# Kernel tuning notes

Hardware: AMD Instinct MI355X
Metric: run time of the kernel (lower is better)

## Reference

```python
import jax, jax.numpy as jnp
import numpy as np
import math

B, T, C = 4, 2048, 1024
N_HEAD = 16
HEAD_DIM = C // N_HEAD


def setup_inputs() -> dict:
    key = jax.random.key(0)
    k1, k2, k3, k4, k5 = jax.random.split(key, 5)
    s = 1.0 / math.sqrt(C)
    return {
        "x": jax.random.normal(k1, (B, T, C), dtype=jnp.float32),
        "W_attn": jax.random.normal(k2, (3 * C, C), dtype=jnp.float32) * s,
        "b_attn": jax.random.normal(k3, (3 * C,), dtype=jnp.float32) * 0.02,
        "W_proj": jax.random.normal(k4, (C, C), dtype=jnp.float32) * s,
        "b_proj": jax.random.normal(k5, (C,), dtype=jnp.float32) * 0.02,
    }


def reference(x, W_attn, b_attn, W_proj, b_proj):
    Bx, Tx, Cx = x.shape
    # QKV projection (torch Linear: x @ W.T + b), split into q,k,v
    qkv = jnp.einsum("btc,dc->btd", x, W_attn) + b_attn  # [B,T,3C]
    q, k, v = jnp.split(qkv, 3, axis=-1)
    # [B,T,C] -> [B,H,T,hd]
    def to_heads(t):
        return t.reshape(Bx, Tx, N_HEAD, HEAD_DIM).transpose(0, 2, 1, 3)
    q, k, v = to_heads(q), to_heads(k), to_heads(v)
    scale = 1.0 / math.sqrt(HEAD_DIM)
    att = jnp.einsum("bhqd,bhkd->bhqk", q, k) * scale  # [B,H,T,T]
    causal = jnp.tril(jnp.ones((Tx, Tx), dtype=bool))
    att = jnp.where(causal, att, -jnp.inf)
    att = jax.nn.softmax(att, axis=-1)
    y = jnp.einsum("bhqk,bhkd->bhqd", att, v)  # [B,H,T,hd]
    y = y.transpose(0, 2, 1, 3).reshape(Bx, Tx, Cx)
    y = jnp.einsum("btc,dc->btd", y, W_proj) + b_proj
    return y
```

## Files before the change

### kernel.cpp

```cpp
#include <hip/hip_runtime.h>
#include <hip/hip_bf16.h>
#include <stdint.h>

typedef unsigned short u16;
typedef __attribute__((ext_vector_type(8))) short bf16x8;
typedef __attribute__((ext_vector_type(4))) short s16x4;
typedef __attribute__((ext_vector_type(4))) float f32x4;

#define B_SZ 4
#define T_SZ 2048
#define C_SZ 1024
#define NH   16
#define HD   64
#define LOG2E 1.44269504088896340736f

__device__ __forceinline__ u16 f2bf(float f) {
  unsigned int u = __float_as_uint(f);
  u += 0x7fffu + ((u >> 16) & 1u);
  return (u16)(u >> 16);
}
__device__ __forceinline__ u16 f2bf_hu(float f) {
  return (u16)((__float_as_uint(f) + 0x8000u) >> 16);
}
__device__ __forceinline__ void gload_lds16(const u16* g, u16* l) {
  __builtin_amdgcn_global_load_lds((const __attribute__((address_space(1))) void*)g,
                                   (__attribute__((address_space(3))) void*)l, 16, 0, 0);
}

__global__ void cast3_f32_bf16(const float* __restrict__ x, const float* __restrict__ wa,
                               const float* __restrict__ wp, u16* __restrict__ xb,
                               u16* __restrict__ wab, u16* __restrict__ wpb) {
  const int n1 = 8192 * 1024 / 8, n2 = 3072 * 1024 / 8, n3 = 1024 * 1024 / 8;
  int i = blockIdx.x * blockDim.x + threadIdx.x;
  const float* in; u16* out; int idx;
  if (i < n1)            { in = x;  out = xb;  idx = i; }
  else if (i < n1 + n2)  { in = wa; out = wab; idx = i - n1; }
  else if (i < n1 + n2 + n3) { in = wp; out = wpb; idx = i - n1 - n2; }
  else return;
  const float4* p = (const float4*)in + (size_t)idx * 2;
  float4 a = p[0], b = p[1];
  bf16x8 o;
  o[0] = (short)f2bf(a.x); o[1] = (short)f2bf(a.y);
  o[2] = (short)f2bf(a.z); o[3] = (short)f2bf(a.w);
  o[4] = (short)f2bf(b.x); o[5] = (short)f2bf(b.y);
  o[6] = (short)f2bf(b.z); o[7] = (short)f2bf(b.w);
  ((bf16x8*)out)[idx] = o;
}

__launch_bounds__(512, 2)
__global__ void gemm8_qkvB(const u16* __restrict__ A, const u16* __restrict__ Bw,
                           const float* __restrict__ bias,
                           u16* __restrict__ O0, u16* __restrict__ O1, u16* __restrict__ O2,
                           int M, int N, int K) {
  extern __shared__ u16 lds[];
  u16* As = lds;
  u16* Bs = lds + 32768;
  const int tid = threadIdx.x;
  const int lane = tid & 63, w = tid >> 6;
  const int wm = w >> 2, wn = w & 3;
  const int quad = lane >> 4, l16 = lane & 15;

  const int gx = gridDim.x;
  const int nwg = gx * gridDim.y;
  const int wg0 = blockIdx.y * gx + blockIdx.x;
  const int swz = (wg0 & 7) * (nwg >> 3) + (wg0 >> 3);
  const int n0 = (swz % gx) * 128;
  const int m0 = (swz / gx) * 256;

  const int dr8 = lane >> 3;
  const int dc8 = (lane & 7) ^ dr8;
  const u16* gAL = A + (size_t)(m0 + w * 8 + dr8) * K + dc8 * 8;
  const u16* gBL = Bw + (size_t)(n0 + w * 8 + dr8) * K + dc8 * 8;
  u16* dA = As + w * 512;
  u16* dB = Bs + w * 512;

  const int NT = K >> 6;

  auto stageA = [&](int tile) {
    u16* d = dA + (tile & 1) * 16384;
    const u16* g = gAL + (size_t)tile * 64;
#pragma unroll
    for (int sg = 0; sg < 4; ++sg)
      gload_lds16(g + (size_t)(sg * 64) * K, d + sg * 4096);
  };
  auto stageB = [&](int tile) {
    u16* d = dB + (tile & 1) * 8192;
    const u16* g = gBL + (size_t)tile * 64;
#pragma unroll
    for (int sg = 0; sg < 2; ++sg)
      gload_lds16(g + (size_t)(sg * 64) * K, d + sg * 4096);
  };

  f32x4 acc[8][2];
#pragma unroll
  for (int i = 0; i < 8; i++)
#pragma unroll
    for (int j = 0; j < 2; j++) acc[i][j] = (f32x4){0.f, 0.f, 0.f, 0.f};

  stageA(0); stageB(0); stageB(1);
  asm volatile("s_waitcnt vmcnt(2)" ::: "memory");
  __builtin_amdgcn_s_barrier();

  const int sK0 = ((quad) ^ (l16 & 7)) * 8;
  const int sK1 = ((4 + quad) ^ (l16 & 7)) * 8;

  for (int tile = 0; tile < NT; ++tile) {
    const u16* Ab = As + (tile & 1) * 16384 + wm * 8192;
    const u16* Bb = Bs + (tile & 1) * 8192 + wn * 2048;
    bf16x8 bfr[2][2];
#pragma unroll
    for (int mp = 0; mp < 2; ++mp) {
      bf16x8 af[4][2];
#pragma unroll
      for (int a = 0; a < 4; ++a) {
        const int ro = ((mp * 4 + a) * 16 + l16) * 64;
        af[a][0] = *(const bf16x8*)&Ab[ro + sK0];
        af[a][1] = *(const bf16x8*)&Ab[ro + sK1];
      }
      if (mp == 0) {
#pragma unroll
        for (int nt = 0; nt < 2; ++nt) {
          const int ro = (nt * 16 + l16) * 64;
          bfr[nt][0] = *(const bf16x8*)&Bb[ro + sK0];
          bfr[nt][1] = *(const bf16x8*)&Bb[ro + sK1];
        }
        if (tile + 1 < NT) stageA(tile + 1);
        asm volatile("s_waitcnt lgkmcnt(8)");
      } else {
        if (tile + 2 < NT) stageB(tile + 2);
        asm volatile("s_waitcnt lgkmcnt(4)");
      }
      asm volatile("" ::: "memory");
      __builtin_amdgcn_s_barrier();
      asm volatile("s_waitcnt lgkmcnt(0)" ::: "memory");
      __builtin_amdgcn_sched_barrier(0);
      __builtin_amdgcn_s_setprio(1);
#pragma unroll
      for (int a = 0; a < 4; ++a)
#pragma unroll
        for (int nt = 0; nt < 2; ++nt) {
          f32x4 c = acc[mp * 4 + a][nt];
          c = __builtin_amdgcn_mfma_f32_16x16x32_bf16(af[a][0], bfr[nt][0], c, 0, 0, 0);
          c = __builtin_amdgcn_mfma_f32_16x16x32_bf16(af[a][1], bfr[nt][1], c, 0, 0, 0);
          acc[mp * 4 + a][nt] = c;
        }
      __builtin_amdgcn_s_setprio(0);
      if (mp == 1) {
        if (tile + 2 >= NT) asm volatile("s_waitcnt vmcnt(0)" ::: "memory");
        else                asm volatile("s_waitcnt vmcnt(2)" ::: "memory");
      }
      asm volatile("" ::: "memory");
      __builtin_amdgcn_s_barrier();
    }
  }

  float bv[2];
#pragma unroll
  for (int nt = 0; nt < 2; nt++) bv[nt] = bias[n0 + wn * 32 + nt * 16 + l16];

  const int ncol = n0 + wn * 32;
  const int nsec = ncol >> 10;
  const int hh = (ncol >> 6) & 15;
  const int dho = ncol & 63;
  if (nsec < 2) {
    u16* dst = (nsec == 0 ? O0 : O1);
#pragma unroll
    for (int mt = 0; mt < 8; mt++) {
      const int row = m0 + wm * 128 + mt * 16 + quad * 4;
      const int bb = row >> 11;
      const int t = row & 2047;
#pragma unroll
      for (int nt = 0; nt < 2; nt++) {
        const int dh = dho + nt * 16 + l16;
        const size_t a = (((size_t)bb * NH + hh) * T_SZ + t) * HD + dh;
#pragma unroll
        for (int r = 0; r < 4; r++)
          dst[a + (size_t)r * HD] = f2bf(acc[mt][nt][r] + bv[nt]);
      }
    }
  } else {
    u16* vth = O2;
    u16* S = lds + (size_t)w * (32 * 136);
#pragma unroll
    for (int mt = 0; mt < 8; ++mt)
#pragma unroll
      for (int nt = 0; nt < 2; ++nt) {
        s16x4 pk;
#pragma unroll
        for (int r = 0; r < 4; ++r) pk[r] = (short)f2bf(acc[mt][nt][r] + bv[nt]);
        *(s16x4*)&S[(nt * 16 + l16) * 136 + mt * 16 + quad * 4] = pk;
      }
    const int tbase = m0 + wm * 128;
    const int bb = tbase >> 11;
    const int tb = tbase & 2047;
    const size_t vrow = ((size_t)bb * NH + hh) * HD;
    const int tc = (lane & 15) * 8;
#pragma unroll
    for (int i = 0; i < 8; ++i) {
      const int nr = i * 4 + (lane >> 4);
      bf16x8 vv = *(const bf16x8*)&S[nr * 136 + tc];
      *(bf16x8*)&vth[(vrow + dho + nr) * T_SZ + tb + tc] = vv;
    }
  }
}

__launch_bounds__(512, 2)
__global__ void gemm8_proj(const u16* __restrict__ A, const u16* __restrict__ Bw,
                           const float* __restrict__ bias, float* __restrict__ Cout,
                           int M, int N, int K) {
  extern __shared__ u16 lds[];
  u16* As = lds;
  u16* Bs = lds + 32768;
  const int tid = threadIdx.x;
  const int lane = tid & 63, w = tid >> 6;
  const int wm = w >> 2, wn = w & 3;
  const int quad = lane >> 4, l16 = lane & 15;

  const int gx = gridDim.x;
  const int nwg = gx * gridDim.y;
  const int wg0 = blockIdx.y * gx + blockIdx.x;
  const int swz = (wg0 & 7) * (nwg >> 3) + (wg0 >> 3);
  const int n0 = (swz % gx) * 128;
  const int m0 = (swz / gx) * 256;

  const int dr8 = lane >> 3;
  const int dc8 = (lane & 7) ^ dr8;
  const u16* gAL = A + (size_t)(m0 + w * 8 + dr8) * K + dc8 * 8;
  const u16* gBL = Bw + (size_t)(n0 + w * 8 + dr8) * K + dc8 * 8;
  u16* dA = As + w * 512;
  u16* dB = Bs + w * 512;

  const int NT = K >> 6;

  auto stageA = [&](int tile) {
    u16* d = dA + (tile & 1) * 16384;
    const u16* g = gAL + (size_t)tile * 64;
#pragma unroll
    for (int sg = 0; sg < 4; ++sg)
      gload_lds16(g + (size_t)(sg * 64) * K, d + sg * 4096);
  };
  auto stageB = [&](int tile) {
    u16* d = dB + (tile & 1) * 8192;
    const u16* g = gBL + (size_t)tile * 64;
#pragma unroll
    for (int sg = 0; sg < 2; ++sg)
      gload_lds16(g + (size_t)(sg * 64) * K, d + sg * 4096);
  };

  f32x4 acc[8][2];
#pragma unroll
  for (int i = 0; i < 8; i++)
#pragma unroll
    for (int j = 0; j < 2; j++) acc[i][j] = (f32x4){0.f, 0.f, 0.f, 0.f};

  stageA(0); stageB(0); stageB(1);
  asm volatile("s_waitcnt vmcnt(2)" ::: "memory");
  __builtin_amdgcn_s_barrier();

  const int sK0 = ((quad) ^ (l16 & 7)) * 8;
  const int sK1 = ((4 + quad) ^ (l16 & 7)) * 8;

  for (int tile = 0; tile < NT; ++tile) {
    const u16* Ab = As + (tile & 1) * 16384 + wm * 8192;
    const u16* Bb = Bs + (tile & 1) * 8192 + wn * 2048;
    bf16x8 bfr[2][2];
#pragma unroll
    for (int mp = 0; mp < 2; ++mp) {
      bf16x8 af[4][2];
#pragma unroll
      for (int a = 0; a < 4; ++a) {
        const int ro = ((mp * 4 + a) * 16 + l16) * 64;
        af[a][0] = *(const bf16x8*)&Ab[ro + sK0];
        af[a][1] = *(const bf16x8*)&Ab[ro + sK1];
      }
      if (mp == 0) {
#pragma unroll
        for (int nt = 0; nt < 2; ++nt) {
          const int ro = (nt * 16 + l16) * 64;
          bfr[nt][0] = *(const bf16x8*)&Bb[ro + sK0];
          bfr[nt][1] = *(const bf16x8*)&Bb[ro + sK1];
        }
        if (tile + 1 < NT) stageA(tile + 1);
        asm volatile("s_waitcnt lgkmcnt(8)");
      } else {
        if (tile + 2 < NT) stageB(tile + 2);
        asm volatile("s_waitcnt lgkmcnt(4)");
      }
      asm volatile("" ::: "memory");
      __builtin_amdgcn_s_barrier();
      asm volatile("s_waitcnt lgkmcnt(0)" ::: "memory");
      __builtin_amdgcn_sched_barrier(0);
      __builtin_amdgcn_s_setprio(1);
#pragma unroll
      for (int a = 0; a < 4; ++a)
#pragma unroll
        for (int nt = 0; nt < 2; ++nt) {
          f32x4 c = acc[mp * 4 + a][nt];
          c = __builtin_amdgcn_mfma_f32_16x16x32_bf16(af[a][0], bfr[nt][0], c, 0, 0, 0);
          c = __builtin_amdgcn_mfma_f32_16x16x32_bf16(af[a][1], bfr[nt][1], c, 0, 0, 0);
          acc[mp * 4 + a][nt] = c;
        }
      __builtin_amdgcn_s_setprio(0);
      if (mp == 1) {
        if (tile + 2 >= NT) asm volatile("s_waitcnt vmcnt(0)" ::: "memory");
        else                asm volatile("s_waitcnt vmcnt(2)" ::: "memory");
      }
      asm volatile("" ::: "memory");
      __builtin_amdgcn_s_barrier();
    }
  }

  float bv[2];
#pragma unroll
  for (int nt = 0; nt < 2; nt++) bv[nt] = bias[n0 + wn * 32 + nt * 16 + l16];
#pragma unroll
  for (int mt = 0; mt < 8; mt++) {
    const int row = m0 + wm * 128 + mt * 16 + quad * 4;
#pragma unroll
    for (int nt = 0; nt < 2; nt++) {
      const int col = n0 + wn * 32 + nt * 16 + l16;
#pragma unroll
      for (int r = 0; r < 4; r++)
        Cout[(size_t)(row + r) * N + col] = acc[mt][nt][r] + bv[nt];
    }
  }
}

__device__ __forceinline__ void attn_step(
    int kb, int kbn, int w, int quad, int l16, int qt128, int sw0, int sw1,
    const u16* gK0, const u16* gK1, const u16* gV0, const u16* gV1,
    u16* KsF, u16* VsF, u16* PsW,
    const bf16x8 (&qf)[2][2], f32x4 (&o)[2][4], float (&l_i)[2][4]) {
  __syncthreads();

  if (kb + 1 < kbn) {
    const int nb = (kb + 1) & 1;
    const size_t ko = (size_t)(kb + 1) * 64 * HD;
    const int vo = (kb + 1) * 64;
    gload_lds16(gK0 + ko, KsF + nb * 4096 + (2 * w) * 512);
    gload_lds16(gK1 + ko, KsF + nb * 4096 + (2 * w + 1) * 512);
    gload_lds16(gV0 + vo, VsF + nb * 4096 + (2 * w) * 512);
    gload_lds16(gV1 + vo, VsF + nb * 4096 + (2 * w + 1) * 512);
  }

  const u16* Kb = KsF + (kb & 1) * 4096;
  const u16* Vb = VsF + (kb & 1) * 4096;
  const int kt0 = kb * 64;
  const float SC = 0.125f * LOG2E;

  f32x4 s[2][4];
  __builtin_amdgcn_s_setprio(1);
#pragma unroll
  for (int nt = 0; nt < 4; nt++) {
    bf16x8 kf0 = *(const bf16x8*)&Kb[(nt * 16 + l16) * 64 + sw0];
    bf16x8 kf1 = *(const bf16x8*)&Kb[(nt * 16 + l16) * 64 + sw1];
#pragma unroll
    for (int m = 0; m < 2; m++) {
      f32x4 t0 = (f32x4){0.f, 0.f, 0.f, 0.f};
      t0 = __builtin_amdgcn_mfma_f32_16x16x32_bf16(qf[m][0], kf0, t0, 0, 0, 0);
      t0 = __builtin_amdgcn_mfma_f32_16x16x32_bf16(qf[m][1], kf1, t0, 0, 0, 0);
      s[m][nt] = t0;
    }
  }
  __builtin_amdgcn_s_setprio(0);

  bf16x8 p0a, p1a, p0b, p1b;
#pragma unroll
  for (int m = 0; m < 2; m++) {
    const int mrow = qt128 + w * 32 + m * 16;
    const int qr = mrow + quad * 4;
    const bool diag = (kt0 + 64 > mrow);

    if (diag) {
#pragma unroll
      for (int nt = 0; nt < 4; nt++) {
        const int dk = kt0 + nt * 16 + l16 - qr;
#pragma unroll
        for (int r = 0; r < 4; r++) {
          float v = (dk > r) ? -10000.f : s[m][nt][r] * SC;
          s[m][nt][r] = exp2f(v);
        }
      }
    } else {
#pragma unroll
      for (int nt = 0; nt < 4; nt++)
#pragma unroll
        for (int r = 0; r < 4; r++)
          s[m][nt][r] = exp2f(s[m][nt][r] * SC);
    }
#pragma unroll
    for (int r = 0; r < 4; r++)
      l_i[m][r] += (s[m][0][r] + s[m][1][r]) + (s[m][2][r] + s[m][3][r]);

#pragma unroll
    for (int nt = 0; nt < 4; nt++)
#pragma unroll
      for (int r = 0; r < 4; r++)
        PsW[(quad * 4 + r) * 72 + nt * 16 + l16] = f2bf_hu(s[m][nt][r]);
    if (m == 0) {
      p0a = *(const bf16x8*)&PsW[l16 * 72 + quad * 8];
      p1a = *(const bf16x8*)&PsW[l16 * 72 + 32 + quad * 8];
    } else {
      p0b = *(const bf16x8*)&PsW[l16 * 72 + quad * 8];
      p1b = *(const bf16x8*)&PsW[l16 * 72 + 32 + quad * 8];
    }
  }

  __builtin_amdgcn_s_setprio(1);
#pragma unroll
  for (int nt = 0; nt < 4; nt++) {
    bf16x8 v0 = *(const bf16x8*)&Vb[(nt * 16 + l16) * 64 + sw0];
    bf16x8 v1 = *(const bf16x8*)&Vb[(nt * 16 + l16) * 64 + sw1];
    o[0][nt] = __builtin_amdgcn_mfma_f32_16x16x32_bf16(p0a, v0, o[0][nt], 0, 0, 0);
    o[0][nt] = __builtin_amdgcn_mfma_f32_16x16x32_bf16(p1a, v1, o[0][nt], 0, 0, 0);
    o[1][nt] = __builtin_amdgcn_mfma_f32_16x16x32_bf16(p0b, v0, o[1][nt], 0, 0, 0);
    o[1][nt] = __builtin_amdgcn_mfma_f32_16x16x32_bf16(p1b, v1, o[1][nt], 0, 0, 0);
  }
  __builtin_amdgcn_s_setprio(0);
}

__launch_bounds__(256, 3)
__global__ void attn_fused(const u16* __restrict__ qh, const u16* __restrict__ kh,
                           const u16* __restrict__ vth, u16* __restrict__ out) {
  __shared__ __align__(16) u16 Ks[2][64 * 64];
  __shared__ __align__(16) u16 Vs[2][64 * 64];
  __shared__ __align__(16) u16 Ps[4][16 * 72];
  const int qt = 15 - blockIdx.z;
  const int h = blockIdx.x, b = blockIdx.y;
  const int tid = threadIdx.x;
  const int lane = tid & 63, w = tid >> 6;
  const int quad = lane >> 4, l16 = lane & 15;
  const size_t bh = (size_t)b * NH + h;
  const u16* Kbase = kh + bh * T_SZ * HD;
  const u16* Vbase = vth + bh * HD * T_SZ;
  const int qt128 = qt * 128;

  const int dr = lane >> 3;
  const int dc = (lane & 7) ^ dr;
  const u16* gK0 = Kbase + (size_t)(2 * w * 8 + dr) * HD + dc * 8;
  const u16* gK1 = Kbase + (size_t)((2 * w + 1) * 8 + dr) * HD + dc * 8;
  const u16* gV0 = Vbase + (size_t)(2 * w * 8 + dr) * T_SZ + dc * 8;
  const u16* gV1 = Vbase + (size_t)((2 * w + 1) * 8 + dr) * T_SZ + dc * 8;
  u16* KsF = &Ks[0][0];
  u16* VsF = &Vs[0][0];
  u16* PsW = &Ps[w][0];

  bf16x8 qf[2][2];
#pragma unroll
  for (int m = 0; m < 2; m++) {
    const int t = qt128 + w * 32 + m * 16 + l16;
    const u16* qrow = qh + (bh * T_SZ + t) * HD;
    qf[m][0] = *(const bf16x8*)(qrow + quad * 8);
    qf[m][1] = *(const bf16x8*)(qrow + 32 + quad * 8);
  }

  f32x4 o[2][4];
  float l_i[2][4];
#pragma unroll
  for (int m = 0; m < 2; m++)
#pragma unroll
    for (int i = 0; i < 4; i++) {
      o[m][i] = (f32x4){0.f, 0.f, 0.f, 0.f};
      l_i[m][i] = 0.f;
    }

  const int kbn = 2 * qt + 2;
  const int sw0 = (quad ^ (l16 & 7)) * 8;
  const int sw1 = ((4 + quad) ^ (l16 & 7)) * 8;

  gload_lds16(gK0, KsF + (2 * w) * 512);
  gload_lds16(gK1, KsF + (2 * w + 1) * 512);
  gload_lds16(gV0, VsF + (2 * w) * 512);
  gload_lds16(gV1, VsF + (2 * w + 1) * 512);

  for (int kb = 0; kb < kbn; kb++)
    attn_step(kb, kbn, w, quad, l16, qt128, sw0, sw1,
              gK0, gK1, gV0, gV1, KsF, VsF, PsW, qf, o, l_i);

#pragma unroll
  for (int m = 0; m < 2; m++)
#pragma unroll
    for (int r = 0; r < 4; r++) {
      float v = l_i[m][r];
      v += __shfl_xor(v, 1);
      v += __shfl_xor(v, 2);
      v += __shfl_xor(v, 4);
      v += __shfl_xor(v, 8);
      const float inv = 1.f / v;
      const int t = qt128 + w * 32 + m * 16 + quad * 4 + r;
      const size_t orow = ((size_t)b * T_SZ + t) * C_SZ + (size_t)h * HD;
#pragma unroll
      for (int nt = 0; nt < 4; nt++)
        out[orow + nt * 16 + l16] = f2bf(o[m][nt][r] * inv);
    }
}

extern "C" void kernel_launch(void* const* d_in, const int* in_sizes, int n_in,
                              void* d_out, int out_size, void* d_ws, size_t ws_size,
                              hipStream_t stream) {
  (void)in_sizes; (void)n_in; (void)out_size; (void)ws_size;
  const float* x      = (const float*)d_in[0];
  const float* W_attn = (const float*)d_in[1];
  const float* b_attn = (const float*)d_in[2];
  const float* W_proj = (const float*)d_in[3];
  const float* b_proj = (const float*)d_in[4];
  float* out = (float*)d_out;

  char* ws = (char*)d_ws;
  u16* xb  = (u16*)ws;  ws += (size_t)8192 * 1024 * 2;
  u16* Wab = (u16*)ws;  ws += (size_t)3072 * 1024 * 2;
  u16* Wpb = (u16*)ws;  ws += (size_t)1024 * 1024 * 2;
  u16* qhb = (u16*)ws;  ws += (size_t)8192 * 1024 * 2;
  u16* khb = (u16*)ws;  ws += (size_t)8192 * 1024 * 2;
  u16* vtb = (u16*)ws;  ws += (size_t)8192 * 1024 * 2;
  u16* aob = (u16*)ws;

  dim3 blk(256);
  cast3_f32_bf16<<<6144, blk, 0, stream>>>(x, W_attn, W_proj, xb, Wab, Wpb);

  gemm8_qkvB<<<dim3(3072 / 128, 8192 / 256), dim3(512), 98304, stream>>>(
      xb, Wab, b_attn, qhb, khb, vtb, 8192, 3072, 1024);
  attn_fused<<<dim3(NH, B_SZ, 16), blk, 0, stream>>>(qhb, khb, vtb, aob);
  gemm8_proj<<<dim3(1024 / 128, 8192 / 256), dim3(512), 98304, stream>>>(
      aob, Wpb, b_proj, out, 8192, 1024, 1024);
}
```

Before: 247.8 us.

## Fold softmax scale into Q projection and transpose QK^T MFMA output

The softmax scale (1/sqrt(hd)·log2e) is now applied once in the QKV projection epilogue when writing Q, which removes a multiply per score element in the attention loop. The QK^T MFMA operands are swapped so each lane holds a key-row slice of scores. That lets the P tile be written to LDS as packed 4-element vector stores instead of scalar stores, and lets the row-sum be a single per-lane scalar reduced with two cross-lane shuffles at the end. Rounding Q to bf16 after scaling changes numerics slightly.

```diff
diff --git a/kernel.cpp b/kernel.cpp
--- a/kernel.cpp
+++ b/kernel.cpp
@@ -164,6 +164,7 @@
   const int dho = ncol & 63;
   if (nsec < 2) {
     u16* dst = (nsec == 0 ? O0 : O1);
+    const float qs = (nsec == 0) ? (0.125f * LOG2E) : 1.0f;
 #pragma unroll
     for (int mt = 0; mt < 8; mt++) {
       const int row = m0 + wm * 128 + mt * 16 + quad * 4;
@@ -175,7 +176,7 @@
         const size_t a = (((size_t)bb * NH + hh) * T_SZ + t) * HD + dh;
 #pragma unroll
         for (int r = 0; r < 4; r++)
-          dst[a + (size_t)r * HD] = f2bf(acc[mt][nt][r] + bv[nt]);
+          dst[a + (size_t)r * HD] = f2bf((acc[mt][nt][r] + bv[nt]) * qs);
       }
     }
   } else {
@@ -330,7 +331,7 @@
     int kb, int kbn, int w, int quad, int l16, int qt128, int sw0, int sw1,
     const u16* gK0, const u16* gK1, const u16* gV0, const u16* gV1,
     u16* KsF, u16* VsF, u16* PsW,
-    const bf16x8 (&qf)[2][2], f32x4 (&o)[2][4], float (&l_i)[2][4]) {
+    const bf16x8 (&qf)[2][2], f32x4 (&o)[2][4], float (&l_i)[2]) {
   __syncthreads();
 
   if (kb + 1 < kbn) {
@@ -346,7 +347,6 @@
   const u16* Kb = KsF + (kb & 1) * 4096;
   const u16* Vb = VsF + (kb & 1) * 4096;
   const int kt0 = kb * 64;
-  const float SC = 0.125f * LOG2E;
 
   f32x4 s[2][4];
   __builtin_amdgcn_s_setprio(1);
@@ -357,27 +357,27 @@
 #pragma unroll
     for (int m = 0; m < 2; m++) {
       f32x4 t0 = (f32x4){0.f, 0.f, 0.f, 0.f};
-      t0 = __builtin_amdgcn_mfma_f32_16x16x32_bf16(qf[m][0], kf0, t0, 0, 0, 0);
-      t0 = __builtin_amdgcn_mfma_f32_16x16x32_bf16(qf[m][1], kf1, t0, 0, 0, 0);
+      t0 = __builtin_amdgcn_mfma_f32_16x16x32_bf16(kf0, qf[m][0], t0, 0, 0, 0);
+      t0 = __builtin_amdgcn_mfma_f32_16x16x32_bf16(kf1, qf[m][1], t0, 0, 0, 0);
       s[m][nt] = t0;
     }
   }
   __builtin_amdgcn_s_setprio(0);
 
+  const int qml = quad * 4 - l16;
   bf16x8 p0a, p1a, p0b, p1b;
 #pragma unroll
   for (int m = 0; m < 2; m++) {
     const int mrow = qt128 + w * 32 + m * 16;
-    const int qr = mrow + quad * 4;
     const bool diag = (kt0 + 64 > mrow);
 
     if (diag) {
 #pragma unroll
       for (int nt = 0; nt < 4; nt++) {
-        const int dk = kt0 + nt * 16 + l16 - qr;
+        const int tt = kt0 + nt * 16 - mrow + qml;
 #pragma unroll
         for (int r = 0; r < 4; r++) {
-          float v = (dk > r) ? -10000.f : s[m][nt][r] * SC;
+          float v = (tt + r > 0) ? -10000.f : s[m][nt][r];
           s[m][nt][r] = exp2f(v);
         }
       }
@@ -386,17 +386,21 @@
       for (int nt = 0; nt < 4; nt++)
 #pragma unroll
         for (int r = 0; r < 4; r++)
-          s[m][nt][r] = exp2f(s[m][nt][r] * SC);
-    }
-#pragma unroll
-    for (int r = 0; r < 4; r++)
-      l_i[m][r] += (s[m][0][r] + s[m][1][r]) + (s[m][2][r] + s[m][3][r]);
-
+          s[m][nt][r] = exp2f(s[m][nt][r]);
+    }
+    float ls = 0.f;
 #pragma unroll
     for (int nt = 0; nt < 4; nt++)
-#pragma unroll
-      for (int r = 0; r < 4; r++)
-        PsW[(quad * 4 + r) * 72 + nt * 16 + l16] = f2bf_hu(s[m][nt][r]);
+      ls += (s[m][nt][0] + s[m][nt][1]) + (s[m][nt][2] + s[m][nt][3]);
+    l_i[m] += ls;
+
+#pragma unroll
+    for (int nt = 0; nt < 4; nt++) {
+      s16x4 pk;
+#pragma unroll
+      for (int r = 0; r < 4; r++) pk[r] = (short)f2bf_hu(s[m][nt][r]);
+      *(s16x4*)&PsW[l16 * 72 + nt * 16 + quad * 4] = pk;
+    }
     if (m == 0) {
       p0a = *(const bf16x8*)&PsW[l16 * 72 + quad * 8];
       p1a = *(const bf16x8*)&PsW[l16 * 72 + 32 + quad * 8];
@@ -455,14 +459,13 @@
   }
 
   f32x4 o[2][4];
-  float l_i[2][4];
-#pragma unroll
-  for (int m = 0; m < 2; m++)
-#pragma unroll
-    for (int i = 0; i < 4; i++) {
-      o[m][i] = (f32x4){0.f, 0.f, 0.f, 0.f};
-      l_i[m][i] = 0.f;
-    }
+  float l_i[2];
+#pragma unroll
+  for (int m = 0; m < 2; m++) {
+    l_i[m] = 0.f;
+#pragma unroll
+    for (int i = 0; i < 4; i++) o[m][i] = (f32x4){0.f, 0.f, 0.f, 0.f};
+  }
 
   const int kbn = 2 * qt + 2;
   const int sw0 = (quad ^ (l16 & 7)) * 8;
@@ -478,21 +481,20 @@
               gK0, gK1, gV0, gV1, KsF, VsF, PsW, qf, o, l_i);
 
 #pragma unroll
-  for (int m = 0; m < 2; m++)
+  for (int m = 0; m < 2; m++) {
+    float v = l_i[m];
+    v += __shfl_xor(v, 16);
+    v += __shfl_xor(v, 32);
 #pragma unroll
     for (int r = 0; r < 4; r++) {
-      float v = l_i[m][r];
-      v += __shfl_xor(v, 1);
-      v += __shfl_xor(v, 2);
-      v += __shfl_xor(v, 4);
-      v += __shfl_xor(v, 8);
-      const float inv = 1.f / v;
+      const float inv = 1.f / __shfl(v, quad * 4 + r);
       const int t = qt128 + w * 32 + m * 16 + quad * 4 + r;
       const size_t orow = ((size_t)b * T_SZ + t) * C_SZ + (size_t)h * HD;
 #pragma unroll
       for (int nt = 0; nt < 4; nt++)
         out[orow + nt * 16 + l16] = f2bf(o[m][nt][r] * inv);
     }
+  }
 }
 
 extern "C" void kernel_launch(void* const* d_in, const int* in_sizes, int n_in,
```

After: 250.9 us. About the same (+1.2%).
